# Optimization experiments

Measured on AMD Instinct MI355X. Metric: run time of the kernel, lower is better.

The kernel has to match this reference:

```python
import jax, jax.numpy as jnp
import numpy as np

B, DIN, H, D, M = 16384, 256, 200, 256, 64
N_ITER = 100


def setup_inputs() -> dict:
    key = jax.random.key(0)
    ks = jax.random.split(key, 8)
    g = lambda k, shape, sc: jax.random.normal(k, shape, jnp.float32) * sc
    return {
        "x": jax.random.normal(ks[0], (B, DIN), jnp.float32),
        "b": 0.1 * jax.random.normal(ks[1], (B, M), jnp.float32),
        "W1": g(ks[2], (DIN, H), 1.0 / np.sqrt(DIN)),
        "b1": jnp.zeros((H,), jnp.float32),
        "W2": g(ks[3], (H, H), 1.0 / np.sqrt(H)),
        "b2": jnp.zeros((H,), jnp.float32),
        "W3": g(ks[4], (H, D), 1.0 / np.sqrt(H)),
        "b3": jnp.zeros((D,), jnp.float32),
        "A": g(ks[5], (M, D), 1.0 / np.sqrt(D)),
        "lb": -jnp.ones((D,), jnp.float32),
        "ub": jnp.ones((D,), jnp.float32),
        "n_iter": N_ITER,
    }


def reference(x, b, W1, b1, W2, b2, W3, b3, A, lb, ub, n_iter):
    sigma, omega = 1.0, 1.7
    # --- MLP trunk ---
    h = jax.nn.relu(x @ W1 + b1)
    h = jax.nn.relu(h @ W2 + b2)
    y = h @ W3 + b3  # [B, D] raw output; also the DR init (get_init)

    # Precompute (A A^T)^{-1} once (M x M, tiny), reused every iteration.
    eye = jnp.eye(A.shape[0], dtype=A.dtype)
    AAT_inv = jnp.linalg.inv(A @ A.T + 1e-6 * eye)

    def P_eq(z):
        # projection onto {z : A z = b}, with sigma relaxation on the correction
        r = z @ A.T - b  # [B, M] residual
        return z - sigma * (r @ AAT_inv) @ A

    def P_box(z):
        return jnp.clip(z, lb, ub)

    # Relaxed Douglas-Rachford / SOR fixed-point iteration, sequential state.
    def body(z, _):
        p = P_box(z)
        q = P_eq(2.0 * p - z)
        return z + omega * (q - p), None

    z, _ = jax.lax.scan(body, y, None, length=n_iter)
    return P_eq(P_box(z))
```

## Files before the change

### kernel.cpp

```cpp
#include <hip/hip_runtime.h>


typedef float f32x4 __attribute__((ext_vector_type(4)));
typedef float f32x16 __attribute__((ext_vector_type(16)));
typedef unsigned u32x4 __attribute__((ext_vector_type(4)));
typedef short short8 __attribute__((ext_vector_type(8)));

__device__ __forceinline__ unsigned pack_hi(float a, float b) {
  return __builtin_amdgcn_perm(__float_as_uint(b), __float_as_uint(a), 0x07060302u);
}
__device__ __forceinline__ float trunch(float x) {
  return __uint_as_float(__float_as_uint(x) & 0xFFFF0000u);
}
__device__ __forceinline__ float med3(float x, float lo, float hi) {
  return __builtin_amdgcn_fmed3f(x, lo, hi);
}
__device__ __forceinline__ void split2x4(f32x4 a, f32x4 b, short8& hi, short8& lo) {
  union { unsigned u[4]; short8 v; } H, L;
  H.u[0] = pack_hi(a[0], a[1]); H.u[1] = pack_hi(a[2], a[3]);
  H.u[2] = pack_hi(b[0], b[1]); H.u[3] = pack_hi(b[2], b[3]);
  float l0 = a[0] - trunch(a[0]), l1 = a[1] - trunch(a[1]);
  float l2 = a[2] - trunch(a[2]), l3 = a[3] - trunch(a[3]);
  float l4 = b[0] - trunch(b[0]), l5 = b[1] - trunch(b[1]);
  float l6 = b[2] - trunch(b[2]), l7 = b[3] - trunch(b[3]);
  L.u[0] = pack_hi(l0, l1); L.u[1] = pack_hi(l2, l3);
  L.u[2] = pack_hi(l4, l5); L.u[3] = pack_hi(l6, l7);
  hi = H.v; lo = L.v;
}
__device__ __forceinline__ f32x4 mfma16(short8 a, short8 b, f32x4 c) {
  return __builtin_amdgcn_mfma_f32_16x16x32_bf16(a, b, c, 0, 0, 0);
}
__device__ __forceinline__ f32x16 mfma32(short8 a, short8 b, f32x16 c) {
  return __builtin_amdgcn_mfma_f32_32x32x16_bf16(a, b, c, 0, 0, 0);
}

__global__ __launch_bounds__(512) void prep_transw(
    const float* __restrict__ A, float* __restrict__ G_out,
    unsigned short* __restrict__ Wtbph, unsigned short* __restrict__ Wtbpl,
    const float* __restrict__ W1, const float* __restrict__ W2,
    const float* __restrict__ W3,
    unsigned short* __restrict__ T1h, unsigned short* __restrict__ T1l,
    unsigned short* __restrict__ T2h, unsigned short* __restrict__ T2l,
    unsigned short* __restrict__ T3h, unsigned short* __restrict__ T3l) {
  const int t = threadIdx.x;
  if (blockIdx.x != 0) {
    const int b = blockIdx.x - 1;
    const float* W; unsigned short *Th, *Tl; int K, N, KP, NP, base;
    if (b < 112)      { W = W1; Th = T1h; Tl = T1l; K = 256; N = 200; KP = 256; NP = 224; base = b; }
    else if (b < 210) { W = W2; Th = T2h; Tl = T2l; K = 200; N = 200; KP = 224; NP = 224; base = b - 112; }
    else              { W = W3; Th = T3h; Tl = T3l; K = 200; N = 256; KP = 224; NP = 256; base = b - 210; }
    int idx = base * 512 + t;
    if (idx >= NP * KP) return;
    int n = idx / KP, k = idx - n * KP;
    float v = (n < N && k < K) ? W[k * N + n] : 0.f;
    unsigned u = __float_as_uint(v);
    Th[idx] = (unsigned short)(u >> 16);
    float lo = v - __uint_as_float(u & 0xFFFF0000u);
    Tl[idx] = (unsigned short)(__float_as_uint(lo) >> 16);
    return;
  }

  __shared__ float As[64 * 260];
  __shared__ float T[64 * 65];
  __shared__ float Xi[64 * 65];

  for (int q = 0; q < 8; ++q) {
    int f = 4 * (t + 512 * q);
    f32x4 v = *(const f32x4*)&A[f];
    int m = f >> 8, d = f & 255;
    *(f32x4*)&As[m * 260 + d] = v;
  }
  __syncthreads();

  for (int q = 0; q < 8; ++q) {
    int f = t + 512 * q;
    int i = f >> 6, j = f & 63;
    float s = 0.f;
    for (int d = 0; d < 256; d += 4) {
      f32x4 xa = *(const f32x4*)&As[i * 260 + d];
      f32x4 xb = *(const f32x4*)&As[j * 260 + d];
      s += xa[0] * xb[0] + xa[1] * xb[1] + xa[2] * xb[2] + xa[3] * xb[3];
    }
    if (i == j) s += 1e-6f;
    T[i * 65 + j] = s;
  }
  __syncthreads();

  if (t < 64) {
    for (int j = 0; j < 64; ++j) {
      float dj = sqrtf(T[j * 65 + j]);
      float lij = 0.f;
      if (t == j) T[j * 65 + j] = dj;
      if (t > j) { lij = T[t * 65 + j] / dj; T[t * 65 + j] = lij; }
      for (int k = j + 1; k <= t; ++k)
        T[t * 65 + k] -= lij * T[k * 65 + j];
    }
    for (int i = 0; i < 64; ++i) {
      float s = (i == t) ? 1.f : 0.f;
      for (int j = t; j < i; ++j) s -= T[i * 65 + j] * Xi[j * 65 + t];
      Xi[i * 65 + t] = (i >= t) ? s / T[i * 65 + i] : 0.f;
    }
    for (int i = 0; i < 64; ++i) {
      float v = Xi[i * 65 + t];
      unsigned u = __float_as_uint(v);
      Wtbph[i * 64 + t] = (unsigned short)(u >> 16);
      float lo = v - __uint_as_float(u & 0xFFFF0000u);
      Wtbpl[i * 64 + t] = (unsigned short)(__float_as_uint(lo) >> 16);
    }
  }
  __syncthreads();

  {
    const int i = t & 63;
    const int grp = t >> 6;
    float xrow[64];
#pragma unroll
    for (int j = 0; j < 64; ++j) xrow[j] = Xi[i * 65 + j];
    for (int c = 0; c < 4; ++c) {
      const int d0 = 8 * grp + 64 * c;
      float acc[8] = {};
#pragma unroll
      for (int j = 0; j < 64; ++j) {
        f32x4 a0 = *(const f32x4*)&As[j * 260 + d0];
        f32x4 a1 = *(const f32x4*)&As[j * 260 + d0 + 4];
        float x = xrow[j];
        acc[0] += x * a0[0]; acc[1] += x * a0[1];
        acc[2] += x * a0[2]; acc[3] += x * a0[3];
        acc[4] += x * a1[0]; acc[5] += x * a1[1];
        acc[6] += x * a1[2]; acc[7] += x * a1[3];
      }
      *(f32x4*)&G_out[i * 256 + d0] = (f32x4){acc[0], acc[1], acc[2], acc[3]};
      *(f32x4*)&G_out[i * 256 + d0 + 4] = (f32x4){acc[4], acc[5], acc[6], acc[7]};
    }
  }
}

__global__ __launch_bounds__(512) void gemm_mfma(
    const float* __restrict__ Af, const unsigned short* __restrict__ Ah,
    const unsigned short* __restrict__ Al, int lda,
    const unsigned short* __restrict__ Wth, const unsigned short* __restrict__ Wtl,
    const float* __restrict__ bias, float* __restrict__ Yf,
    unsigned short* __restrict__ Yh, unsigned short* __restrict__ Yl,
    int ldout, int N, int NP, int ksteps, int relu) {
  __shared__ __align__(16) unsigned short Xh_s[32][40], Xl_s[32][40];
  __shared__ __align__(16) unsigned short Wh_s[256][40], Wl_s[256][40];

  const int t = threadIdx.x, wv = t >> 6, lane = t & 63;
  const int lhi = lane >> 4, llo = lane & 15;
  const int row0 = blockIdx.x * 32;
  const int ntiles = NP >> 4;
  const int KPw = ksteps * 32;
  const int srow = t >> 2, sk8 = (t & 3) * 8;
  const int wn = t >> 1, wh = (t & 1) * 16;

  f32x4 acc[2][2];
#pragma unroll
  for (int mt = 0; mt < 2; ++mt)
#pragma unroll
    for (int i = 0; i < 2; ++i) acc[mt][i] = (f32x4){0.f, 0.f, 0.f, 0.f};

  for (int kc = 0; kc < ksteps; ++kc) {
    const int k0 = kc * 32;
    if (kc) __syncthreads();
    if (t < 128) {
      if (Af) {
        f32x4 v0 = *(const f32x4*)&Af[(size_t)(row0 + srow) * lda + k0 + sk8];
        f32x4 v1 = *(const f32x4*)&Af[(size_t)(row0 + srow) * lda + k0 + sk8 + 4];
        short8 hv, lv;
        split2x4(v0, v1, hv, lv);
        *(short8*)&Xh_s[srow][sk8] = hv;
        *(short8*)&Xl_s[srow][sk8] = lv;
      } else {
        *(short8*)&Xh_s[srow][sk8] = *(const short8*)&Ah[(size_t)(row0 + srow) * lda + k0 + sk8];
        *(short8*)&Xl_s[srow][sk8] = *(const short8*)&Al[(size_t)(row0 + srow) * lda + k0 + sk8];
      }
    }
    if (wn < NP) {
      const u32x4* sh = (const u32x4*)&Wth[(size_t)wn * KPw + k0 + wh];
      const u32x4* sl = (const u32x4*)&Wtl[(size_t)wn * KPw + k0 + wh];
      u32x4 h0 = sh[0], h1 = sh[1], l0 = sl[0], l1 = sl[1];
      *(u32x4*)&Wh_s[wn][wh] = h0; *(u32x4*)&Wh_s[wn][wh + 8] = h1;
      *(u32x4*)&Wl_s[wn][wh] = l0; *(u32x4*)&Wl_s[wn][wh + 8] = l1;
    }
    __syncthreads();
    short8 Axh[2], Axl[2];
#pragma unroll
    for (int mt = 0; mt < 2; ++mt) {
      Axh[mt] = *(const short8*)&Xh_s[16 * mt + llo][8 * lhi];
      Axl[mt] = *(const short8*)&Xl_s[16 * mt + llo][8 * lhi];
    }
#pragma unroll
    for (int i = 0; i < 2; ++i) {
      int nt = wv + 8 * i;
      if (nt < ntiles) {
        short8 Bh = *(const short8*)&Wh_s[16 * nt + llo][8 * lhi];
        short8 Bl = *(const short8*)&Wl_s[16 * nt + llo][8 * lhi];
#pragma unroll
        for (int mt = 0; mt < 2; ++mt) {
          acc[mt][i] = mfma16(Axh[mt], Bh, acc[mt][i]);
          acc[mt][i] = mfma16(Axl[mt], Bh, acc[mt][i]);
          acc[mt][i] = mfma16(Axh[mt], Bl, acc[mt][i]);
        }
      }
    }
  }

#pragma unroll
  for (int i = 0; i < 2; ++i) {
    int nt = wv + 8 * i;
    if (nt >= ntiles) continue;
    int col = 16 * nt + llo;
    float bv = (bias && col < N) ? bias[col] : 0.f;
#pragma unroll
    for (int mt = 0; mt < 2; ++mt) {
      f32x4 c = acc[mt][i];
      int rowb = row0 + 16 * mt + 4 * lhi;
#pragma unroll
      for (int reg = 0; reg < 4; ++reg) {
        float v = c[reg] + bv;
        if (relu) v = fmaxf(v, 0.f);
        if (col >= N) v = 0.f;
        if (Yf) {
          if (col < N) Yf[(size_t)(rowb + reg) * ldout + col] = v;
        } else {
          unsigned u = __float_as_uint(v);
          float lo = v - __uint_as_float(u & 0xFFFF0000u);
          Yh[(size_t)(rowb + reg) * ldout + col] = (unsigned short)(u >> 16);
          Yl[(size_t)(rowb + reg) * ldout + col] =
              (unsigned short)(__float_as_uint(lo) >> 16);
        }
      }
    }
  }
}

__global__ __launch_bounds__(256) __attribute__((amdgpu_waves_per_eu(2, 2)))
void iter_kernel(const float* __restrict__ y0,
                 const float* __restrict__ Gg,
                 const float* __restrict__ bMg,
                 const unsigned short* __restrict__ Wtbph,
                 const unsigned short* __restrict__ Wtbpl,
                 const float* __restrict__ lb,
                 const float* __restrict__ ub,
                 const int* __restrict__ n_iter_p,
                 float* __restrict__ out) {
  __shared__ __align__(16) float wbuf[32 * 256];
  __shared__ __align__(16) float part[4 * 32 * 68];
  __shared__ __align__(16) unsigned rs[2 * 32 * 32];

  const int t = threadIdx.x, wv = t >> 6, lane = t & 63;
  const int l31 = lane & 31, h = lane >> 5;
  const int lhi = lane >> 4, llo = lane & 15;
  const int R0 = blockIdx.x * 32;
  const int n_iter = n_iter_p[0];

  f32x4 bcc[2];
  bcc[0] = (f32x4){0.f, 0.f, 0.f, 0.f};
  bcc[1] = (f32x4){0.f, 0.f, 0.f, 0.f};
#pragma unroll
  for (int ks = 0; ks < 2; ++ks) {
    short8 Bh = *(const short8*)&Wtbph[(16 * wv + llo) * 64 + 32 * ks + 8 * lhi];
    short8 Bl = *(const short8*)&Wtbpl[(16 * wv + llo) * 64 + 32 * ks + 8 * lhi];
#pragma unroll
    for (int mt = 0; mt < 2; ++mt) {
      const float* ap = &bMg[(size_t)(R0 + 16 * mt + llo) * 64 + 32 * ks + 8 * lhi];
      short8 Ah_, Al_;
      split2x4(*(const f32x4*)ap, *(const f32x4*)(ap + 4), Ah_, Al_);
      bcc[mt] = mfma16(Ah_, Bh, bcc[mt]);
      bcc[mt] = mfma16(Al_, Bh, bcc[mt]);
      bcc[mt] = mfma16(Ah_, Bl, bcc[mt]);
    }
  }
#pragma unroll
  for (int mt = 0; mt < 2; ++mt)
#pragma unroll
    for (int reg = 0; reg < 4; ++reg)
      part[(16 * mt + 4 * lhi + reg) * 64 + 16 * wv + llo] = bcc[mt][reg];
  __syncthreads();
  const int rrow = t >> 3, m8 = (t & 7) * 8;
  f32x4 bpr0 = *(const f32x4*)&part[rrow * 64 + m8];
  f32x4 bpr1 = *(const f32x4*)&part[rrow * 64 + m8 + 4];

  short8 GAh[2][4], GAl[2][4];
#pragma unroll
  for (int mt = 0; mt < 2; ++mt)
#pragma unroll
    for (int ks = 0; ks < 4; ++ks) {
      const float* gp = &Gg[(32 * mt + l31) * 256 + 64 * wv + 16 * ks + 8 * h];
      split2x4(*(const f32x4*)gp, *(const f32x4*)(gp + 4), GAh[mt][ks], GAl[mt][ks]);
    }
  short8 GBh[4][2], GBl[4][2];
#pragma unroll
  for (int td = 0; td < 4; ++td)
#pragma unroll
    for (int ks2 = 0; ks2 < 2; ++ks2) {
      f32x4 fa, fb;
#pragma unroll
      for (int j = 0; j < 4; ++j) {
        fa[j] = Gg[(32 * ks2 + 8 * lhi + j) * 256 + 64 * wv + 16 * td + llo];
        fb[j] = Gg[(32 * ks2 + 8 * lhi + 4 + j) * 256 + 64 * wv + 16 * td + llo];
      }
      split2x4(fa, fb, GBh[td][ks2], GBl[td][ks2]);
    }

  f32x4 lbr[4], ubr[4];
#pragma unroll
  for (int td = 0; td < 4; ++td) {
    lbr[td] = *(const f32x4*)&lb[64 * wv + 16 * td + 4 * lhi];
    ubr[td] = *(const f32x4*)&ub[64 * wv + 16 * td + 4 * lhi];
  }

  int waddr[2][4];
  {
    int r3 = llo & 7;
#pragma unroll
    for (int tr = 0; tr < 2; ++tr)
#pragma unroll
      for (int td = 0; td < 4; ++td)
        waddr[tr][td] = (16 * tr + llo) * 1024 + 16 * (((16 * wv + 4 * td + lhi) ^ r3));
  }
  int raddr[4];
  {
    int r3 = l31 & 7;
#pragma unroll
    for (int ks = 0; ks < 4; ++ks)
      raddr[ks] = l31 * 1024 + 16 * ((16 * wv + 4 * ks + 2 * h) ^ r3);
  }
  const int pbase = ((wv * 32 + l31) * 68 + 4 * h) * 4;
  const int prd = (rrow * 68 + m8) * 4;
  const int rwr = rrow * 128 + 16 * ((t & 7) ^ (rrow & 7));
  int rrd[2][2];
  {
    int r3 = llo & 7;
#pragma unroll
    for (int tr = 0; tr < 2; ++tr)
#pragma unroll
      for (int ks2 = 0; ks2 < 2; ++ks2)
        rrd[tr][ks2] = (16 * tr + llo) * 128 + 16 * ((4 * ks2 + lhi) ^ r3);
  }

  f32x4 z[4][2];
#pragma unroll
  for (int tr = 0; tr < 2; ++tr)
#pragma unroll
    for (int td = 0; td < 4; ++td) {
      f32x4 v = *(const f32x4*)&y0[(R0 + 16 * tr + llo) * 256 + 64 * wv + 16 * td + 4 * lhi];
      z[td][tr] = v;
      f32x4 wq;
#pragma unroll
      for (int e = 0; e < 4; ++e) {
        float p = med3(v[e], lbr[td][e], ubr[td][e]);
        wq[e] = (n_iter == 0) ? p : fmaf(2.f, p, -v[e]);
      }
      *(f32x4*)((char*)wbuf + waddr[tr][td]) = wq;
    }
  __syncthreads();

  for (int it = 0; it <= n_iter; ++it) {
    f32x16 acc0 = {}, acc1 = {};
#pragma unroll
    for (int ks = 0; ks < 4; ++ks) {
      f32x4 f0 = *(const f32x4*)((const char*)wbuf + raddr[ks]);
      f32x4 f1 = *(const f32x4*)((const char*)wbuf + (raddr[ks] ^ 16));
      short8 Bh, Bl;
      split2x4(f0, f1, Bh, Bl);
      __builtin_amdgcn_s_setprio(1);
      acc0 = mfma32(GAh[0][ks], Bh, acc0);
      acc0 = mfma32(GAh[0][ks], Bl, acc0);
      acc0 = mfma32(GAl[0][ks], Bh, acc0);
      acc1 = mfma32(GAh[1][ks], Bh, acc1);
      acc1 = mfma32(GAh[1][ks], Bl, acc1);
      acc1 = mfma32(GAl[1][ks], Bh, acc1);
      __builtin_amdgcn_s_setprio(0);
    }
#pragma unroll
    for (int u = 0; u < 4; ++u) {
      f32x4 q0 = {acc0[4 * u], acc0[4 * u + 1], acc0[4 * u + 2], acc0[4 * u + 3]};
      f32x4 q1 = {acc1[4 * u], acc1[4 * u + 1], acc1[4 * u + 2], acc1[4 * u + 3]};
      *(f32x4*)((char*)part + (pbase + 32 * u)) = q0;
      *(f32x4*)((char*)part + (pbase + 32 * u + 128)) = q1;
    }
    __syncthreads();

    {
      const char* pb = (const char*)part + prd;
      f32x4 s0 = *(const f32x4*)pb;
      f32x4 s1 = *(const f32x4*)(pb + 16);
      s0 += *(const f32x4*)(pb + 8704);  s1 += *(const f32x4*)(pb + 8720);
      s0 += *(const f32x4*)(pb + 17408); s1 += *(const f32x4*)(pb + 17424);
      s0 += *(const f32x4*)(pb + 26112); s1 += *(const f32x4*)(pb + 26128);
      s0 -= bpr0; s1 -= bpr1;
      u32x4 hi4 = {pack_hi(s0[0], s0[1]), pack_hi(s0[2], s0[3]),
                   pack_hi(s1[0], s1[1]), pack_hi(s1[2], s1[3])};
      float l0 = s0[0] - trunch(s0[0]), l1 = s0[1] - trunch(s0[1]);
      float l2 = s0[2] - trunch(s0[2]), l3 = s0[3] - trunch(s0[3]);
      float l4 = s1[0] - trunch(s1[0]), l5 = s1[1] - trunch(s1[1]);
      float l6 = s1[2] - trunch(s1[2]), l7 = s1[3] - trunch(s1[3]);
      u32x4 lo4 = {pack_hi(l0, l1), pack_hi(l2, l3), pack_hi(l4, l5), pack_hi(l6, l7)};
      *(u32x4*)((char*)rs + rwr) = hi4;
      *(u32x4*)((char*)rs + (rwr + 4096)) = lo4;
    }
    __syncthreads();

#pragma unroll
    for (int tr = 0; tr < 2; ++tr) {
      short8 Rh[2], Rl[2];
#pragma unroll
      for (int ks2 = 0; ks2 < 2; ++ks2) {
        Rh[ks2] = *(const short8*)((const char*)rs + rrd[tr][ks2]);
        Rl[ks2] = *(const short8*)((const char*)rs + (rrd[tr][ks2] + 4096));
      }
      f32x4 c[4];
      __builtin_amdgcn_s_setprio(1);
#pragma unroll
      for (int td = 0; td < 4; ++td) {
        f32x4 cc = {};
        cc = mfma16(GBh[td][0], Rh[0], cc);
        cc = mfma16(GBh[td][0], Rl[0], cc);
        cc = mfma16(GBl[td][0], Rh[0], cc);
        cc = mfma16(GBh[td][1], Rh[1], cc);
        cc = mfma16(GBh[td][1], Rl[1], cc);
        cc = mfma16(GBl[td][1], Rh[1], cc);
        c[td] = cc;
      }
      __builtin_amdgcn_s_setprio(0);

      if (it < n_iter - 1) {
#pragma unroll
        for (int td = 0; td < 4; ++td) {
          f32x4 zz = z[td][tr], zn, wq;
#pragma unroll
          for (int e = 0; e < 4; ++e) {
            float p = med3(zz[e], lbr[td][e], ubr[td][e]);
            zn[e] = fmaf(1.7f, p - zz[e] - c[td][e], zz[e]);
            float pn = med3(zn[e], lbr[td][e], ubr[td][e]);
            wq[e] = fmaf(2.f, pn, -zn[e]);
          }
          z[td][tr] = zn;
          *(f32x4*)((char*)wbuf + waddr[tr][td]) = wq;
        }
      } else if (it == n_iter - 1) {
#pragma unroll
        for (int td = 0; td < 4; ++td) {
          f32x4 zz = z[td][tr], zn, wq;
#pragma unroll
          for (int e = 0; e < 4; ++e) {
            float p = med3(zz[e], lbr[td][e], ubr[td][e]);
            zn[e] = fmaf(1.7f, p - zz[e] - c[td][e], zz[e]);
            wq[e] = med3(zn[e], lbr[td][e], ubr[td][e]);
          }
          z[td][tr] = zn;
          *(f32x4*)((char*)wbuf + waddr[tr][td]) = wq;
        }
      } else {
#pragma unroll
        for (int td = 0; td < 4; ++td) {
          f32x4 zz = z[td][tr], o;
#pragma unroll
          for (int e = 0; e < 4; ++e) {
            float p = med3(zz[e], lbr[td][e], ubr[td][e]);
            o[e] = p - c[td][e];
          }
          *(f32x4*)&out[(R0 + 16 * tr + llo) * 256 + 64 * wv + 16 * td + 4 * lhi] = o;
        }
      }
    }
  }
}

extern "C" void kernel_launch(void* const* d_in, const int* in_sizes, int n_in,
                              void* d_out, int out_size, void* d_ws, size_t ws_size,
                              hipStream_t stream) {
  (void)in_sizes; (void)n_in; (void)out_size; (void)ws_size;
  const float* x  = (const float*)d_in[0];
  const float* bM = (const float*)d_in[1];
  const float* W1 = (const float*)d_in[2];
  const float* b1 = (const float*)d_in[3];
  const float* W2 = (const float*)d_in[4];
  const float* b2 = (const float*)d_in[5];
  const float* W3 = (const float*)d_in[6];
  const float* b3 = (const float*)d_in[7];
  const float* A  = (const float*)d_in[8];
  const float* lb = (const float*)d_in[9];
  const float* ub = (const float*)d_in[10];
  const int* n_iter = (const int*)d_in[11];
  float* out = (float*)d_out;

  char* ws = (char*)d_ws;
  unsigned short* H1h  = (unsigned short*)(ws + 0);
  unsigned short* H1l  = (unsigned short*)(ws + 7340032);
  unsigned short* H2h  = (unsigned short*)(ws + 14680064);
  unsigned short* H2l  = (unsigned short*)(ws + 22020096);
  float*          G    = (float*)(ws + 29360128);
  unsigned short* Wt1h = (unsigned short*)(ws + 29425664);
  unsigned short* Wt1l = (unsigned short*)(ws + 29540352);
  unsigned short* Wt2h = (unsigned short*)(ws + 29655040);
  unsigned short* Wt2l = (unsigned short*)(ws + 29755392);
  unsigned short* Wt3h = (unsigned short*)(ws + 29855744);
  unsigned short* Wt3l = (unsigned short*)(ws + 29970432);
  unsigned short* Wtbph = (unsigned short*)(ws + 30085120);
  unsigned short* Wtbpl = (unsigned short*)(ws + 30093312);
  float* y = out;

  hipLaunchKernelGGL(prep_transw, dim3(323), dim3(512), 0, stream,
                     A, G, Wtbph, Wtbpl, W1, W2, W3,
                     Wt1h, Wt1l, Wt2h, Wt2l, Wt3h, Wt3l);

  hipLaunchKernelGGL(gemm_mfma, dim3(512), dim3(512), 0, stream,
                     x, (const unsigned short*)nullptr, (const unsigned short*)nullptr, 256,
                     Wt1h, Wt1l, b1, (float*)nullptr, H1h, H1l, 224, 200, 224, 8, 1);
  hipLaunchKernelGGL(gemm_mfma, dim3(512), dim3(512), 0, stream,
                     (const float*)nullptr, H1h, H1l, 224,
                     Wt2h, Wt2l, b2, (float*)nullptr, H2h, H2l, 224, 200, 224, 7, 1);
  hipLaunchKernelGGL(gemm_mfma, dim3(512), dim3(512), 0, stream,
                     (const float*)nullptr, H2h, H2l, 224,
                     Wt3h, Wt3l, b3, y, (unsigned short*)nullptr, (unsigned short*)nullptr,
                     256, 256, 256, 7, 0);

  hipLaunchKernelGGL(iter_kernel, dim3(512), dim3(256), 0, stream,
                     y, G, bM, Wtbph, Wtbpl, lb, ub, n_iter, out);
}
```

Before: 579.9 us.

## Replace serial Cholesky inverse with parallel Newton-Schulz and drop b-precompute

```diff
diff --git a/kernel.cpp b/kernel.cpp
--- a/kernel.cpp
+++ b/kernel.cpp
@@ -35,8 +35,7 @@
 }
 
 __global__ __launch_bounds__(512) void prep_transw(
-    const float* __restrict__ A, float* __restrict__ G_out,
-    unsigned short* __restrict__ Wtbph, unsigned short* __restrict__ Wtbpl,
+    const float* __restrict__ A, float* __restrict__ HAg,
     const float* __restrict__ W1, const float* __restrict__ W2,
     const float* __restrict__ W3,
     unsigned short* __restrict__ T1h, unsigned short* __restrict__ T1l,
@@ -61,8 +60,9 @@
   }
 
   __shared__ float As[64 * 260];
-  __shared__ float T[64 * 65];
-  __shared__ float Xi[64 * 65];
+  __shared__ float Ms[64 * 68];
+  __shared__ float Xb[64 * 68], Yb[64 * 68], Zb[64 * 68];
+  __shared__ float nrm[64];
 
   for (int q = 0; q < 8; ++q) {
     int f = 4 * (t + 512 * q);
@@ -82,40 +82,71 @@
       s += xa[0] * xb[0] + xa[1] * xb[1] + xa[2] * xb[2] + xa[3] * xb[3];
     }
     if (i == j) s += 1e-6f;
-    T[i * 65 + j] = s;
+    Ms[i * 68 + j] = s;
   }
   __syncthreads();
 
   if (t < 64) {
-    for (int j = 0; j < 64; ++j) {
-      float dj = sqrtf(T[j * 65 + j]);
-      float lij = 0.f;
-      if (t == j) T[j * 65 + j] = dj;
-      if (t > j) { lij = T[t * 65 + j] / dj; T[t * 65 + j] = lij; }
-      for (int k = j + 1; k <= t; ++k)
-        T[t * 65 + k] -= lij * T[k * 65 + j];
-    }
-    for (int i = 0; i < 64; ++i) {
-      float s = (i == t) ? 1.f : 0.f;
-      for (int j = t; j < i; ++j) s -= T[i * 65 + j] * Xi[j * 65 + t];
-      Xi[i * 65 + t] = (i >= t) ? s / T[i * 65 + i] : 0.f;
-    }
-    for (int i = 0; i < 64; ++i) {
-      float v = Xi[i * 65 + t];
-      unsigned u = __float_as_uint(v);
-      Wtbph[i * 64 + t] = (unsigned short)(u >> 16);
-      float lo = v - __uint_as_float(u & 0xFFFF0000u);
-      Wtbpl[i * 64 + t] = (unsigned short)(__float_as_uint(lo) >> 16);
-    }
+    float s = 0.f;
+    for (int j = 0; j < 64; ++j) s += fabsf(Ms[t * 68 + j]);
+    nrm[t] = s;
   }
   __syncthreads();
+  float mx = 0.f;
+#pragma unroll
+  for (int j = 0; j < 64; ++j) mx = fmaxf(mx, nrm[j]);
+  const float alpha = 1.0f / mx;
+
+  const int ri = t >> 3, j0 = (t & 7) * 8;
+#pragma unroll
+  for (int e = 0; e < 8; ++e) Xb[ri * 68 + j0 + e] = (ri == j0 + e) ? alpha : 0.f;
+  __syncthreads();
+
+  float* Xp = Xb;
+  float* Zp = Zb;
+  for (int itn = 0; itn < 12; ++itn) {
+    f32x4 a0 = {0.f, 0.f, 0.f, 0.f}, a1 = {0.f, 0.f, 0.f, 0.f};
+    for (int k4 = 0; k4 < 16; ++k4) {
+      f32x4 mv = *(const f32x4*)&Ms[ri * 68 + 4 * k4];
+#pragma unroll
+      for (int e = 0; e < 4; ++e) {
+        int k = 4 * k4 + e;
+        f32x4 x0 = *(const f32x4*)&Xp[k * 68 + j0];
+        f32x4 x1 = *(const f32x4*)&Xp[k * 68 + j0 + 4];
+        a0 += mv[e] * x0;
+        a1 += mv[e] * x1;
+      }
+    }
+    *(f32x4*)&Yb[ri * 68 + j0] = a0;
+    *(f32x4*)&Yb[ri * 68 + j0 + 4] = a1;
+    __syncthreads();
+    a0 = (f32x4){0.f, 0.f, 0.f, 0.f};
+    a1 = (f32x4){0.f, 0.f, 0.f, 0.f};
+    for (int k4 = 0; k4 < 16; ++k4) {
+      f32x4 xv = *(const f32x4*)&Xp[ri * 68 + 4 * k4];
+#pragma unroll
+      for (int e = 0; e < 4; ++e) {
+        int k = 4 * k4 + e;
+        f32x4 y0 = *(const f32x4*)&Yb[k * 68 + j0];
+        f32x4 y1 = *(const f32x4*)&Yb[k * 68 + j0 + 4];
+        a0 += xv[e] * y0;
+        a1 += xv[e] * y1;
+      }
+    }
+    f32x4 x0 = *(const f32x4*)&Xp[ri * 68 + j0];
+    f32x4 x1 = *(const f32x4*)&Xp[ri * 68 + j0 + 4];
+    *(f32x4*)&Zp[ri * 68 + j0] = 2.f * x0 - a0;
+    *(f32x4*)&Zp[ri * 68 + j0 + 4] = 2.f * x1 - a1;
+    __syncthreads();
+    float* tmp = Xp; Xp = Zp; Zp = tmp;
+  }
 
   {
     const int i = t & 63;
     const int grp = t >> 6;
-    float xrow[64];
-#pragma unroll
-    for (int j = 0; j < 64; ++j) xrow[j] = Xi[i * 65 + j];
+    float hrow[64];
+#pragma unroll
+    for (int j = 0; j < 64; ++j) hrow[j] = Xp[i * 68 + j];
     for (int c = 0; c < 4; ++c) {
       const int d0 = 8 * grp + 64 * c;
       float acc[8] = {};
@@ -123,14 +154,14 @@
       for (int j = 0; j < 64; ++j) {
         f32x4 a0 = *(const f32x4*)&As[j * 260 + d0];
         f32x4 a1 = *(const f32x4*)&As[j * 260 + d0 + 4];
-        float x = xrow[j];
+        float x = hrow[j];
         acc[0] += x * a0[0]; acc[1] += x * a0[1];
         acc[2] += x * a0[2]; acc[3] += x * a0[3];
         acc[4] += x * a1[0]; acc[5] += x * a1[1];
         acc[6] += x * a1[2]; acc[7] += x * a1[3];
       }
-      *(f32x4*)&G_out[i * 256 + d0] = (f32x4){acc[0], acc[1], acc[2], acc[3]};
-      *(f32x4*)&G_out[i * 256 + d0 + 4] = (f32x4){acc[4], acc[5], acc[6], acc[7]};
+      *(f32x4*)&HAg[i * 256 + d0] = (f32x4){acc[0], acc[1], acc[2], acc[3]};
+      *(f32x4*)&HAg[i * 256 + d0 + 4] = (f32x4){acc[4], acc[5], acc[6], acc[7]};
     }
   }
 }
@@ -236,10 +267,9 @@
 
 __global__ __launch_bounds__(256) __attribute__((amdgpu_waves_per_eu(2, 2)))
 void iter_kernel(const float* __restrict__ y0,
-                 const float* __restrict__ Gg,
+                 const float* __restrict__ Ag,
+                 const float* __restrict__ HAg,
                  const float* __restrict__ bMg,
-                 const unsigned short* __restrict__ Wtbph,
-                 const unsigned short* __restrict__ Wtbpl,
                  const float* __restrict__ lb,
                  const float* __restrict__ ub,
                  const int* __restrict__ n_iter_p,
@@ -254,39 +284,12 @@
   const int R0 = blockIdx.x * 32;
   const int n_iter = n_iter_p[0];
 
-  f32x4 bcc[2];
-  bcc[0] = (f32x4){0.f, 0.f, 0.f, 0.f};
-  bcc[1] = (f32x4){0.f, 0.f, 0.f, 0.f};
-#pragma unroll
-  for (int ks = 0; ks < 2; ++ks) {
-    short8 Bh = *(const short8*)&Wtbph[(16 * wv + llo) * 64 + 32 * ks + 8 * lhi];
-    short8 Bl = *(const short8*)&Wtbpl[(16 * wv + llo) * 64 + 32 * ks + 8 * lhi];
-#pragma unroll
-    for (int mt = 0; mt < 2; ++mt) {
-      const float* ap = &bMg[(size_t)(R0 + 16 * mt + llo) * 64 + 32 * ks + 8 * lhi];
-      short8 Ah_, Al_;
-      split2x4(*(const f32x4*)ap, *(const f32x4*)(ap + 4), Ah_, Al_);
-      bcc[mt] = mfma16(Ah_, Bh, bcc[mt]);
-      bcc[mt] = mfma16(Al_, Bh, bcc[mt]);
-      bcc[mt] = mfma16(Ah_, Bl, bcc[mt]);
-    }
-  }
+  short8 GAh[2][4], GAl[2][4];
 #pragma unroll
   for (int mt = 0; mt < 2; ++mt)
 #pragma unroll
-    for (int reg = 0; reg < 4; ++reg)
-      part[(16 * mt + 4 * lhi + reg) * 64 + 16 * wv + llo] = bcc[mt][reg];
-  __syncthreads();
-  const int rrow = t >> 3, m8 = (t & 7) * 8;
-  f32x4 bpr0 = *(const f32x4*)&part[rrow * 64 + m8];
-  f32x4 bpr1 = *(const f32x4*)&part[rrow * 64 + m8 + 4];
-
-  short8 GAh[2][4], GAl[2][4];
-#pragma unroll
-  for (int mt = 0; mt < 2; ++mt)
-#pragma unroll
     for (int ks = 0; ks < 4; ++ks) {
-      const float* gp = &Gg[(32 * mt + l31) * 256 + 64 * wv + 16 * ks + 8 * h];
+      const float* gp = &Ag[(32 * mt + l31) * 256 + 64 * wv + 16 * ks + 8 * h];
       split2x4(*(const f32x4*)gp, *(const f32x4*)(gp + 4), GAh[mt][ks], GAl[mt][ks]);
     }
   short8 GBh[4][2], GBl[4][2];
@@ -297,8 +300,8 @@
       f32x4 fa, fb;
 #pragma unroll
       for (int j = 0; j < 4; ++j) {
-        fa[j] = Gg[(32 * ks2 + 8 * lhi + j) * 256 + 64 * wv + 16 * td + llo];
-        fb[j] = Gg[(32 * ks2 + 8 * lhi + 4 + j) * 256 + 64 * wv + 16 * td + llo];
+        fa[j] = HAg[(32 * ks2 + 8 * lhi + j) * 256 + 64 * wv + 16 * td + llo];
+        fb[j] = HAg[(32 * ks2 + 8 * lhi + 4 + j) * 256 + 64 * wv + 16 * td + llo];
       }
       split2x4(fa, fb, GBh[td][ks2], GBl[td][ks2]);
     }
@@ -309,6 +312,9 @@
     lbr[td] = *(const f32x4*)&lb[64 * wv + 16 * td + 4 * lhi];
     ubr[td] = *(const f32x4*)&ub[64 * wv + 16 * td + 4 * lhi];
   }
+  const int rrow = t >> 3, m8 = (t & 7) * 8;
+  f32x4 bpr0 = *(const f32x4*)&bMg[(size_t)(R0 + rrow) * 64 + m8];
+  f32x4 bpr1 = *(const f32x4*)&bMg[(size_t)(R0 + rrow) * 64 + m8 + 4];
 
   int waddr[2][4];
   {
@@ -491,19 +497,17 @@
   unsigned short* H1l  = (unsigned short*)(ws + 7340032);
   unsigned short* H2h  = (unsigned short*)(ws + 14680064);
   unsigned short* H2l  = (unsigned short*)(ws + 22020096);
-  float*          G    = (float*)(ws + 29360128);
+  float*          HA   = (float*)(ws + 29360128);
   unsigned short* Wt1h = (unsigned short*)(ws + 29425664);
   unsigned short* Wt1l = (unsigned short*)(ws + 29540352);
   unsigned short* Wt2h = (unsigned short*)(ws + 29655040);
   unsigned short* Wt2l = (unsigned short*)(ws + 29755392);
   unsigned short* Wt3h = (unsigned short*)(ws + 29855744);
   unsigned short* Wt3l = (unsigned short*)(ws + 29970432);
-  unsigned short* Wtbph = (unsigned short*)(ws + 30085120);
-  unsigned short* Wtbpl = (unsigned short*)(ws + 30093312);
   float* y = out;
 
   hipLaunchKernelGGL(prep_transw, dim3(323), dim3(512), 0, stream,
-                     A, G, Wtbph, Wtbpl, W1, W2, W3,
+                     A, HA, W1, W2, W3,
                      Wt1h, Wt1l, Wt2h, Wt2l, Wt3h, Wt3l);
 
   hipLaunchKernelGGL(gemm_mfma, dim3(512), dim3(512), 0, stream,
@@ -518,5 +522,5 @@
                      256, 256, 256, 7, 0);
 
   hipLaunchKernelGGL(iter_kernel, dim3(512), dim3(256), 0, stream,
-                     y, G, bM, Wtbph, Wtbpl, lb, ub, n_iter, out);
-}
+                     y, A, HA, bM, lb, ub, n_iter, out);
+}
```

Result: faster. 480.6 us (-17.1%).
